# Kernel tuning notes

Measured on AMD Instinct MI355X. Metric: run time of the kernel, lower is better.

## Reference

```python
import jax, jax.numpy as jnp
import numpy as np

B, S, F, D, M = 2, 512, 16384, 768, 262144  # batch, seq, n_features, d_model, n_connections


def setup_inputs() -> dict:
    key = jax.random.key(0)
    k1, k2, k3, k4, k5 = jax.random.split(key, 5)
    up_facts = jax.random.normal(k1, (B, S, F), dtype=jnp.float32)
    down_encoder = jax.random.normal(k2, (F, D), dtype=jnp.float32) * 0.02
    up_decoder = jax.random.normal(k3, (D, F), dtype=jnp.float32) * 0.02
    i_indices = jnp.sort(jax.random.randint(k4, (M,), 0, F, dtype=jnp.int32)).astype(jnp.int64)
    j_indices = jax.random.randint(k5, (M,), 0, F, dtype=jnp.int32).astype(jnp.int64)
    return {
        "up_facts": up_facts,
        "down_encoder": down_encoder,
        "up_decoder": up_decoder,
        "i_indices": i_indices,
        "j_indices": j_indices,
    }


def reference(up_facts, down_encoder, up_decoder, i_indices, j_indices):
    # Virtual weight value for each sparse connection (i -> j):
    #   values[m] = <down_encoder[i_m, :], up_decoder[:, j_m]>
    values = jnp.sum(down_encoder[i_indices] * up_decoder[:, j_indices].T, axis=1)  # [M]
    # Gather upstream feature activations for each connection, scale by value.
    scaled = up_facts[:, :, j_indices] * values  # [B, S, M]
    # Scatter-add into downstream feature slots (duplicate i indices accumulate).
    contributions = jnp.zeros((up_facts.shape[0], up_facts.shape[1], down_encoder.shape[0]),
                              dtype=up_facts.dtype)
    return contributions.at[:, :, i_indices].add(scaled)  # [B, S, F]
```

## Files before the change

### kernel.cpp

```cpp
#include <hip/hip_runtime.h>
#include <hip/hip_bf16.h>

#define D_DIM 768
#define F_DIM 16384
#define M_CONN 262144
#define N_ROWS 1024

__device__ __forceinline__ float bf2f(unsigned short u) {
    return __uint_as_float(((unsigned int)u) << 16);
}

__global__ __launch_bounds__(256) void transpose_v4(const float* __restrict__ in,
                                                    float* __restrict__ out,
                                                    int R, int C) {
    __shared__ float tile[64][66];
    const int t = threadIdx.x;
    const int x0 = blockIdx.x * 64;
    const int y0 = blockIdx.y * 64;
#pragma unroll
    for (int k = 0; k < 4; ++k) {
        const int idx = k * 256 + t;
        const int r = idx >> 4, c4 = idx & 15;
        const float4 v = *(const float4*)(in + (size_t)(y0 + r) * C + x0 + c4 * 4);
        float* p = &tile[r][c4 * 4];
        *(float2*)(p)     = make_float2(v.x, v.y);
        *(float2*)(p + 2) = make_float2(v.z, v.w);
    }
    __syncthreads();
#pragma unroll
    for (int k = 0; k < 4; ++k) {
        const int idx = k * 256 + t;
        const int c = idx >> 4, r4 = idx & 15;
        float4 o;
        o.x = tile[r4 * 4 + 0][c];
        o.y = tile[r4 * 4 + 1][c];
        o.z = tile[r4 * 4 + 2][c];
        o.w = tile[r4 * 4 + 3][c];
        *(float4*)(out + (size_t)(x0 + c) * R + y0 + r4 * 4) = o;
    }
}

__global__ __launch_bounds__(256) void transpose_f2b_v4(const float* __restrict__ in,
                                                        unsigned short* __restrict__ out,
                                                        int R, int C) {
    __shared__ float tile[64][66];
    const int t = threadIdx.x;
    const int x0 = blockIdx.x * 64;
    const int y0 = blockIdx.y * 64;
#pragma unroll
    for (int k = 0; k < 4; ++k) {
        const int idx = k * 256 + t;
        const int r = idx >> 4, c4 = idx & 15;
        const float4 v = *(const float4*)(in + (size_t)(y0 + r) * C + x0 + c4 * 4);
        float* p = &tile[r][c4 * 4];
        *(float2*)(p)     = make_float2(v.x, v.y);
        *(float2*)(p + 2) = make_float2(v.z, v.w);
    }
    __syncthreads();
#pragma unroll
    for (int k = 0; k < 4; ++k) {
        const int idx = k * 256 + t;
        const int c = idx >> 4, r4 = idx & 15;
        __hip_bfloat16 b0 = __float2bfloat16(tile[r4 * 4 + 0][c]);
        __hip_bfloat16 b1 = __float2bfloat16(tile[r4 * 4 + 1][c]);
        __hip_bfloat16 b2 = __float2bfloat16(tile[r4 * 4 + 2][c]);
        __hip_bfloat16 b3 = __float2bfloat16(tile[r4 * 4 + 3][c]);
        ushort4 o;
        o.x = *(unsigned short*)&b0;
        o.y = *(unsigned short*)&b1;
        o.z = *(unsigned short*)&b2;
        o.w = *(unsigned short*)&b3;
        *(ushort4*)(out + (size_t)(x0 + c) * R + y0 + r4 * 4) = o;
    }
}

__global__ __launch_bounds__(256) void values_kernel(const float* __restrict__ de,
                                                     const unsigned short* __restrict__ udT,
                                                     const int* __restrict__ i_idx,
                                                     const int* __restrict__ j_idx,
                                                     float* __restrict__ values) {
    const int wave = (blockIdx.x * blockDim.x + threadIdx.x) >> 6;
    const int lane = threadIdx.x & 63;
    const int mbase = wave * 4;
    int cur_i = -1;
    float4 a0, a1, a2;
#pragma unroll
    for (int t = 0; t < 4; ++t) {
        const int m = mbase + t;
        const int i = i_idx[m];
        const int j = j_idx[m];
        if (i != cur_i) {
            const float4* a = (const float4*)(de + (size_t)i * D_DIM);
            a0 = a[lane]; a1 = a[lane + 64]; a2 = a[lane + 128];
            cur_i = i;
        }
        const ushort4* b = (const ushort4*)(udT + (size_t)j * D_DIM);
        ushort4 u0 = b[lane], u1 = b[lane + 64], u2 = b[lane + 128];
        float s = 0.f;
        s = fmaf(a0.x, bf2f(u0.x), s); s = fmaf(a0.y, bf2f(u0.y), s);
        s = fmaf(a0.z, bf2f(u0.z), s); s = fmaf(a0.w, bf2f(u0.w), s);
        s = fmaf(a1.x, bf2f(u1.x), s); s = fmaf(a1.y, bf2f(u1.y), s);
        s = fmaf(a1.z, bf2f(u1.z), s); s = fmaf(a1.w, bf2f(u1.w), s);
        s = fmaf(a2.x, bf2f(u2.x), s); s = fmaf(a2.y, bf2f(u2.y), s);
        s = fmaf(a2.z, bf2f(u2.z), s); s = fmaf(a2.w, bf2f(u2.w), s);
#pragma unroll
        for (int off = 32; off > 0; off >>= 1)
            s += __shfl_down(s, off, 64);
        if (lane == 0) values[m] = s;
    }
}

__global__ __launch_bounds__(256) void seg_kernel(const int* __restrict__ i_idx,
                                                  int* __restrict__ seg) {
    const int i = blockIdx.x * blockDim.x + threadIdx.x;
    if (i > F_DIM) return;
    if (i == F_DIM) { seg[i] = M_CONN; return; }
    int lo = 0, hi = M_CONN;
    while (lo < hi) {
        int mid = (lo + hi) >> 1;
        if (i_idx[mid] < i) lo = mid + 1; else hi = mid;
    }
    seg[i] = lo;
}

__global__ __launch_bounds__(256) void spmm_kernel(const unsigned short* __restrict__ upT,
                                                   const int* __restrict__ j_idx,
                                                   const float* __restrict__ vals,
                                                   const int* __restrict__ seg,
                                                   float* __restrict__ outT) {
    const int i = blockIdx.x;
    const int t = threadIdx.x;
    const int ms = seg[i], me = seg[i + 1];
    float4 acc0 = make_float4(0.f, 0.f, 0.f, 0.f);
    float4 acc1 = make_float4(0.f, 0.f, 0.f, 0.f);
    int m = ms;
    for (; m + 1 < me; m += 2) {
        const int j0 = j_idx[m], j1 = j_idx[m + 1];
        const float v0 = vals[m], v1 = vals[m + 1];
        const ushort4 x0 = ((const ushort4*)(upT + (size_t)j0 * N_ROWS))[t];
        const ushort4 x1 = ((const ushort4*)(upT + (size_t)j1 * N_ROWS))[t];
        acc0.x = fmaf(v0, bf2f(x0.x), acc0.x); acc0.y = fmaf(v0, bf2f(x0.y), acc0.y);
        acc0.z = fmaf(v0, bf2f(x0.z), acc0.z); acc0.w = fmaf(v0, bf2f(x0.w), acc0.w);
        acc1.x = fmaf(v1, bf2f(x1.x), acc1.x); acc1.y = fmaf(v1, bf2f(x1.y), acc1.y);
        acc1.z = fmaf(v1, bf2f(x1.z), acc1.z); acc1.w = fmaf(v1, bf2f(x1.w), acc1.w);
    }
    if (m < me) {
        const int j0 = j_idx[m];
        const float v0 = vals[m];
        const ushort4 x0 = ((const ushort4*)(upT + (size_t)j0 * N_ROWS))[t];
        acc0.x = fmaf(v0, bf2f(x0.x), acc0.x); acc0.y = fmaf(v0, bf2f(x0.y), acc0.y);
        acc0.z = fmaf(v0, bf2f(x0.z), acc0.z); acc0.w = fmaf(v0, bf2f(x0.w), acc0.w);
    }
    acc0.x += acc1.x; acc0.y += acc1.y; acc0.z += acc1.z; acc0.w += acc1.w;
    ((float4*)(outT + (size_t)i * N_ROWS))[t] = acc0;
}

extern "C" void kernel_launch(void* const* d_in, const int* in_sizes, int n_in,
                              void* d_out, int out_size, void* d_ws, size_t ws_size,
                              hipStream_t stream) {
    const float* up_facts = (const float*)d_in[0];
    const float* de       = (const float*)d_in[1];
    const float* ud       = (const float*)d_in[2];
    const int*   i_idx    = (const int*)d_in[3];
    const int*   j_idx    = (const int*)d_in[4];
    float* out = (float*)d_out;

    char* ws = (char*)d_ws;
    unsigned short* udT = (unsigned short*)ws;
    float* outT   = (float*)ws;
    float* values = (float*)(ws + (size_t)64 * 1024 * 1024);
    int*   seg    = (int*)  (ws + (size_t)65 * 1024 * 1024);
    unsigned short* upT = (unsigned short*)out;

    transpose_f2b_v4<<<dim3(F_DIM / 64, D_DIM / 64), 256, 0, stream>>>(
        ud, udT, D_DIM, F_DIM);
    values_kernel<<<(M_CONN / 4) * 64 / 256, 256, 0, stream>>>(de, udT, i_idx, j_idx, values);
    transpose_f2b_v4<<<dim3(F_DIM / 64, N_ROWS / 64), 256, 0, stream>>>(
        up_facts, upT, N_ROWS, F_DIM);
    seg_kernel<<<(F_DIM + 1 + 255) / 256, 256, 0, stream>>>(i_idx, seg);
    spmm_kernel<<<F_DIM, 256, 0, stream>>>(upT, j_idx, values, seg, outT);
    transpose_v4<<<dim3(N_ROWS / 64, F_DIM / 64), 256, 0, stream>>>(
        outT, out, F_DIM, N_ROWS);
}
```

Measured before the change: 347.9 us.

## Add nontemporal loads/stores, batch gathers in values kernel, unroll spmm by four

The transposes now use nontemporal loads and stores for their streaming input and output, and the spmm output store is also nontemporal. In the values kernel, all index and udT gather loads are issued before any arithmetic so more memory requests are in flight at once. The spmm loop is unrolled from two to four connections with separate accumulators, adding memory-level parallelism at the cost of more registers.

```diff
diff --git a/kernel.cpp b/kernel.cpp
--- a/kernel.cpp
+++ b/kernel.cpp
@@ -5,6 +5,8 @@
 #define F_DIM 16384
 #define M_CONN 262144
 #define N_ROWS 1024
+
+typedef float f32x4 __attribute__((ext_vector_type(4)));
 
 __device__ __forceinline__ float bf2f(unsigned short u) {
     return __uint_as_float(((unsigned int)u) << 16);
@@ -21,22 +23,22 @@
     for (int k = 0; k < 4; ++k) {
         const int idx = k * 256 + t;
         const int r = idx >> 4, c4 = idx & 15;
-        const float4 v = *(const float4*)(in + (size_t)(y0 + r) * C + x0 + c4 * 4);
+        const f32x4 v = __builtin_nontemporal_load(
+            (const f32x4*)(in + (size_t)(y0 + r) * C + x0 + c4 * 4));
         float* p = &tile[r][c4 * 4];
-        *(float2*)(p)     = make_float2(v.x, v.y);
-        *(float2*)(p + 2) = make_float2(v.z, v.w);
+        p[0] = v.x; p[1] = v.y; p[2] = v.z; p[3] = v.w;
     }
     __syncthreads();
 #pragma unroll
     for (int k = 0; k < 4; ++k) {
         const int idx = k * 256 + t;
         const int c = idx >> 4, r4 = idx & 15;
-        float4 o;
+        f32x4 o;
         o.x = tile[r4 * 4 + 0][c];
         o.y = tile[r4 * 4 + 1][c];
         o.z = tile[r4 * 4 + 2][c];
         o.w = tile[r4 * 4 + 3][c];
-        *(float4*)(out + (size_t)(x0 + c) * R + y0 + r4 * 4) = o;
+        __builtin_nontemporal_store(o, (f32x4*)(out + (size_t)(x0 + c) * R + y0 + r4 * 4));
     }
 }
 
@@ -51,10 +53,10 @@
     for (int k = 0; k < 4; ++k) {
         const int idx = k * 256 + t;
         const int r = idx >> 4, c4 = idx & 15;
-        const float4 v = *(const float4*)(in + (size_t)(y0 + r) * C + x0 + c4 * 4);
+        const f32x4 v = __builtin_nontemporal_load(
+            (const f32x4*)(in + (size_t)(y0 + r) * C + x0 + c4 * 4));
         float* p = &tile[r][c4 * 4];
-        *(float2*)(p)     = make_float2(v.x, v.y);
-        *(float2*)(p + 2) = make_float2(v.z, v.w);
+        p[0] = v.x; p[1] = v.y; p[2] = v.z; p[3] = v.w;
     }
     __syncthreads();
 #pragma unroll
@@ -82,31 +84,41 @@
     const int wave = (blockIdx.x * blockDim.x + threadIdx.x) >> 6;
     const int lane = threadIdx.x & 63;
     const int mbase = wave * 4;
+
+    int ii[4], jj[4];
+#pragma unroll
+    for (int t = 0; t < 4; ++t) {
+        ii[t] = i_idx[mbase + t];
+        jj[t] = j_idx[mbase + t];
+    }
+    ushort4 u[4][3];
+#pragma unroll
+    for (int t = 0; t < 4; ++t) {
+        const ushort4* b = (const ushort4*)(udT + (size_t)jj[t] * D_DIM);
+        u[t][0] = b[lane]; u[t][1] = b[lane + 64]; u[t][2] = b[lane + 128];
+    }
+
     int cur_i = -1;
     float4 a0, a1, a2;
 #pragma unroll
     for (int t = 0; t < 4; ++t) {
-        const int m = mbase + t;
-        const int i = i_idx[m];
-        const int j = j_idx[m];
+        const int i = ii[t];
         if (i != cur_i) {
             const float4* a = (const float4*)(de + (size_t)i * D_DIM);
             a0 = a[lane]; a1 = a[lane + 64]; a2 = a[lane + 128];
             cur_i = i;
         }
-        const ushort4* b = (const ushort4*)(udT + (size_t)j * D_DIM);
-        ushort4 u0 = b[lane], u1 = b[lane + 64], u2 = b[lane + 128];
         float s = 0.f;
-        s = fmaf(a0.x, bf2f(u0.x), s); s = fmaf(a0.y, bf2f(u0.y), s);
-        s = fmaf(a0.z, bf2f(u0.z), s); s = fmaf(a0.w, bf2f(u0.w), s);
-        s = fmaf(a1.x, bf2f(u1.x), s); s = fmaf(a1.y, bf2f(u1.y), s);
-        s = fmaf(a1.z, bf2f(u1.z), s); s = fmaf(a1.w, bf2f(u1.w), s);
-        s = fmaf(a2.x, bf2f(u2.x), s); s = fmaf(a2.y, bf2f(u2.y), s);
-        s = fmaf(a2.z, bf2f(u2.z), s); s = fmaf(a2.w, bf2f(u2.w), s);
+        s = fmaf(a0.x, bf2f(u[t][0].x), s); s = fmaf(a0.y, bf2f(u[t][0].y), s);
+        s = fmaf(a0.z, bf2f(u[t][0].z), s); s = fmaf(a0.w, bf2f(u[t][0].w), s);
+        s = fmaf(a1.x, bf2f(u[t][1].x), s); s = fmaf(a1.y, bf2f(u[t][1].y), s);
+        s = fmaf(a1.z, bf2f(u[t][1].z), s); s = fmaf(a1.w, bf2f(u[t][1].w), s);
+        s = fmaf(a2.x, bf2f(u[t][2].x), s); s = fmaf(a2.y, bf2f(u[t][2].y), s);
+        s = fmaf(a2.z, bf2f(u[t][2].z), s); s = fmaf(a2.w, bf2f(u[t][2].w), s);
 #pragma unroll
         for (int off = 32; off > 0; off >>= 1)
             s += __shfl_down(s, off, 64);
-        if (lane == 0) values[m] = s;
+        if (lane == 0) values[mbase + t] = s;
     }
 }
 
@@ -133,26 +145,40 @@
     const int ms = seg[i], me = seg[i + 1];
     float4 acc0 = make_float4(0.f, 0.f, 0.f, 0.f);
     float4 acc1 = make_float4(0.f, 0.f, 0.f, 0.f);
+    float4 acc2 = make_float4(0.f, 0.f, 0.f, 0.f);
+    float4 acc3 = make_float4(0.f, 0.f, 0.f, 0.f);
     int m = ms;
-    for (; m + 1 < me; m += 2) {
-        const int j0 = j_idx[m], j1 = j_idx[m + 1];
-        const float v0 = vals[m], v1 = vals[m + 1];
+    for (; m + 3 < me; m += 4) {
+        const int j0 = j_idx[m],     j1 = j_idx[m + 1];
+        const int j2 = j_idx[m + 2], j3 = j_idx[m + 3];
+        const float v0 = vals[m],     v1 = vals[m + 1];
+        const float v2 = vals[m + 2], v3 = vals[m + 3];
         const ushort4 x0 = ((const ushort4*)(upT + (size_t)j0 * N_ROWS))[t];
         const ushort4 x1 = ((const ushort4*)(upT + (size_t)j1 * N_ROWS))[t];
+        const ushort4 x2 = ((const ushort4*)(upT + (size_t)j2 * N_ROWS))[t];
+        const ushort4 x3 = ((const ushort4*)(upT + (size_t)j3 * N_ROWS))[t];
         acc0.x = fmaf(v0, bf2f(x0.x), acc0.x); acc0.y = fmaf(v0, bf2f(x0.y), acc0.y);
         acc0.z = fmaf(v0, bf2f(x0.z), acc0.z); acc0.w = fmaf(v0, bf2f(x0.w), acc0.w);
         acc1.x = fmaf(v1, bf2f(x1.x), acc1.x); acc1.y = fmaf(v1, bf2f(x1.y), acc1.y);
         acc1.z = fmaf(v1, bf2f(x1.z), acc1.z); acc1.w = fmaf(v1, bf2f(x1.w), acc1.w);
-    }
-    if (m < me) {
+        acc2.x = fmaf(v2, bf2f(x2.x), acc2.x); acc2.y = fmaf(v2, bf2f(x2.y), acc2.y);
+        acc2.z = fmaf(v2, bf2f(x2.z), acc2.z); acc2.w = fmaf(v2, bf2f(x2.w), acc2.w);
+        acc3.x = fmaf(v3, bf2f(x3.x), acc3.x); acc3.y = fmaf(v3, bf2f(x3.y), acc3.y);
+        acc3.z = fmaf(v3, bf2f(x3.z), acc3.z); acc3.w = fmaf(v3, bf2f(x3.w), acc3.w);
+    }
+    for (; m < me; ++m) {
         const int j0 = j_idx[m];
         const float v0 = vals[m];
         const ushort4 x0 = ((const ushort4*)(upT + (size_t)j0 * N_ROWS))[t];
         acc0.x = fmaf(v0, bf2f(x0.x), acc0.x); acc0.y = fmaf(v0, bf2f(x0.y), acc0.y);
         acc0.z = fmaf(v0, bf2f(x0.z), acc0.z); acc0.w = fmaf(v0, bf2f(x0.w), acc0.w);
     }
-    acc0.x += acc1.x; acc0.y += acc1.y; acc0.z += acc1.z; acc0.w += acc1.w;
-    ((float4*)(outT + (size_t)i * N_ROWS))[t] = acc0;
+    f32x4 r;
+    r.x = (acc0.x + acc1.x) + (acc2.x + acc3.x);
+    r.y = (acc0.y + acc1.y) + (acc2.y + acc3.y);
+    r.z = (acc0.z + acc1.z) + (acc2.z + acc3.z);
+    r.w = (acc0.w + acc1.w) + (acc2.w + acc3.w);
+    __builtin_nontemporal_store(r, (f32x4*)(outT + (size_t)i * N_ROWS) + t);
 }
 
 extern "C" void kernel_launch(void* const* d_in, const int* in_sizes, int n_in,
```

Result: no change. 343.2 us (-1.3%).
